# Kernel tuning notes

Hardware: AMD Instinct MI355X
Metric: run time of the kernel (lower is better)

Reference implementation:

```python
import jax, jax.numpy as jnp
import numpy as np

N_IN = 100000
N_OUT = 200000
C_IN = 128
C_OUT = 64
K = 27  # 3x3x3 kernel offsets
M = 100000  # neighbor-map pairs per kernel offset
BN_EPS = 1e-5


def setup_inputs() -> dict:
    key = jax.random.key(0)
    k1, k2, k3, k4 = jax.random.split(key, 4)
    x = jax.random.normal(k1, (N_IN, C_IN), dtype=jnp.float32)
    weight = jax.random.normal(k2, (K, C_IN, C_OUT), dtype=jnp.float32) * (1.0 / np.sqrt(C_IN * K))
    gamma = jnp.ones((C_OUT,), dtype=jnp.float32)
    beta = jnp.zeros((C_OUT,), dtype=jnp.float32)
    in_map = jax.random.randint(k3, (K, M), 0, N_IN, dtype=jnp.int32)
    out_map = jax.random.randint(k4, (K, M), 0, N_OUT, dtype=jnp.int32)
    return {"x": x, "weight": weight, "gamma": gamma, "beta": beta,
            "in_map": in_map, "out_map": out_map}


def sparse_transposed_conv(x, weight, in_map, out_map):
    # gather-GEMM-scatter over K kernel offsets (torchsparse semantics)
    out = jnp.zeros((N_OUT, C_OUT), dtype=x.dtype)

    def body(k, out):
        gathered = x[in_map[k]]                # [M, C_in] irregular gather
        contrib = gathered @ weight[k]         # [M, C_out] small GEMM
        return out.at[out_map[k]].add(contrib) # irregular scatter-add

    return jax.lax.fori_loop(0, K, body, out)


def reference(x, weight, gamma, beta, in_map, out_map):
    out = sparse_transposed_conv(x, weight, in_map, out_map)
    # BatchNorm over points (training-mode batch statistics, biased var)
    mean = jnp.mean(out, axis=0)
    var = jnp.mean(jnp.square(out - mean), axis=0)
    y = (out - mean) * (gamma * jax.lax.rsqrt(var + BN_EPS)) + beta
    return jnp.maximum(y, 0.0)  # ReLU
```

## Files before the change

### kernel.cpp

```cpp
#include <hip/hip_runtime.h>

#define N_IN   100000
#define N_OUT  200000
#define C_IN   128
#define C_OUT  64
#define NK     27
#define MM     100000
#define BN_EPS 1e-5f

#define TILE_M 128
#define APAD   136

typedef short bf16x8 __attribute__((ext_vector_type(8)));
typedef float f32x4  __attribute__((ext_vector_type(4)));

__device__ __forceinline__ unsigned pack2_bf16(float a, float b) {
  unsigned ua = __float_as_uint(a);
  unsigned ub = __float_as_uint(b);
  ua = (ua + 0x7FFFu + ((ua >> 16) & 1u)) >> 16;
  ub = (ub + 0x7FFFu + ((ub >> 16) & 1u)) & 0xFFFF0000u;
  return ua | ub;
}

__global__ void convert_wt_kernel(const float* __restrict__ w, unsigned* __restrict__ wt) {
  int pidx = blockIdx.x * 256 + threadIdx.x;
  int k   = pidx >> 12;
  int rem = pidx & 4095;
  int co  = rem >> 6;
  int ci0 = (rem & 63) * 2;
  const float* wk = w + (size_t)k * C_IN * C_OUT;
  float a = wk[ci0 * C_OUT + co];
  float b = wk[(ci0 + 1) * C_OUT + co];
  wt[pidx] = pack2_bf16(a, b);
}

__global__ __launch_bounds__(256) void scatter_kernel(
    const float* __restrict__ x,
    const unsigned short* __restrict__ wt,
    const int* __restrict__ in_map,
    const int* __restrict__ out_map,
    float* __restrict__ out)
{
  __shared__ unsigned short Als[TILE_M * APAD];
  __shared__ unsigned short Bls[C_OUT * APAD];
  __shared__ int om[TILE_M];

  const int t = threadIdx.x;
  const int k = blockIdx.y;
  const int mbase = blockIdx.x * TILE_M;

  if (t < TILE_M) {
    int m = mbase + t;
    om[t] = (m < MM) ? out_map[k * MM + m] : 0;
  }

  {
    const uint4* src = (const uint4*)(wt + (size_t)k * C_OUT * C_IN);
    #pragma unroll
    for (int i = 0; i < 4; ++i) {
      int ch  = t + i * 256;
      int co  = ch >> 4;
      int ci0 = (ch & 15) * 8;
      *(uint4*)&Bls[co * APAD + ci0] = src[ch];
    }
  }

  {
    int r    = t >> 1;
    int half = t & 1;
    int m    = mbase + r;
    int src  = (m < MM) ? in_map[k * MM + m] : 0;
    const float4* xr = (const float4*)(x + (size_t)src * C_IN) + half * 16;
    uint2* dst = (uint2*)&Als[r * APAD + half * 64];
    #pragma unroll
    for (int j = 0; j < 16; ++j) {
      float4 v = xr[j];
      dst[j] = make_uint2(pack2_bf16(v.x, v.y), pack2_bf16(v.z, v.w));
    }
  }
  __syncthreads();

  const int wave = t >> 6;
  const int lane = t & 63;
  const int quad = lane >> 4;
  const int l15  = lane & 15;
  const int rb   = wave * 32;

  f32x4 acc[2][4];
  #pragma unroll
  for (int i = 0; i < 2; ++i)
    #pragma unroll
    for (int j = 0; j < 4; ++j)
      acc[i][j] = (f32x4){0.f, 0.f, 0.f, 0.f};

  #pragma unroll
  for (int kk = 0; kk < 4; ++kk) {
    const int koff = kk * 32 + quad * 8;
    bf16x8 a0 = *(const bf16x8*)&Als[(rb + l15) * APAD + koff];
    bf16x8 a1 = *(const bf16x8*)&Als[(rb + 16 + l15) * APAD + koff];
    bf16x8 b0 = *(const bf16x8*)&Bls[(l15) * APAD + koff];
    bf16x8 b1 = *(const bf16x8*)&Bls[(16 + l15) * APAD + koff];
    bf16x8 b2 = *(const bf16x8*)&Bls[(32 + l15) * APAD + koff];
    bf16x8 b3 = *(const bf16x8*)&Bls[(48 + l15) * APAD + koff];
    acc[0][0] = __builtin_amdgcn_mfma_f32_16x16x32_bf16(a0, b0, acc[0][0], 0, 0, 0);
    acc[0][1] = __builtin_amdgcn_mfma_f32_16x16x32_bf16(a0, b1, acc[0][1], 0, 0, 0);
    acc[0][2] = __builtin_amdgcn_mfma_f32_16x16x32_bf16(a0, b2, acc[0][2], 0, 0, 0);
    acc[0][3] = __builtin_amdgcn_mfma_f32_16x16x32_bf16(a0, b3, acc[0][3], 0, 0, 0);
    acc[1][0] = __builtin_amdgcn_mfma_f32_16x16x32_bf16(a1, b0, acc[1][0], 0, 0, 0);
    acc[1][1] = __builtin_amdgcn_mfma_f32_16x16x32_bf16(a1, b1, acc[1][1], 0, 0, 0);
    acc[1][2] = __builtin_amdgcn_mfma_f32_16x16x32_bf16(a1, b2, acc[1][2], 0, 0, 0);
    acc[1][3] = __builtin_amdgcn_mfma_f32_16x16x32_bf16(a1, b3, acc[1][3], 0, 0, 0);
  }

  #pragma unroll
  for (int rt = 0; rt < 2; ++rt) {
    int rloc = rb + rt * 16 + quad * 4;
    int4 o4 = *(const int4*)&om[rloc];
    int mrow = mbase + rloc;
    #pragma unroll
    for (int ct = 0; ct < 4; ++ct) {
      f32x4 v = acc[rt][ct];
      int col = ct * 16 + l15;
      if (mrow + 0 < MM) unsafeAtomicAdd(&out[(size_t)o4.x * C_OUT + col], v[0]);
      if (mrow + 1 < MM) unsafeAtomicAdd(&out[(size_t)o4.y * C_OUT + col], v[1]);
      if (mrow + 2 < MM) unsafeAtomicAdd(&out[(size_t)o4.z * C_OUT + col], v[2]);
      if (mrow + 3 < MM) unsafeAtomicAdd(&out[(size_t)o4.w * C_OUT + col], v[3]);
    }
  }
}

__global__ void stats_kernel(const float* __restrict__ out, float* __restrict__ ws) {
  __shared__ float ls[4][64];
  __shared__ float ls2[4][64];
  int t = threadIdx.x;
  int c = t & 63, sub = t >> 6;
  float s = 0.f, s2 = 0.f;
  for (int r = blockIdx.x * 4 + sub; r < N_OUT; r += gridDim.x * 4) {
    float v = out[(size_t)r * C_OUT + c];
    s += v; s2 += v * v;
  }
  ls[sub][c] = s; ls2[sub][c] = s2;
  __syncthreads();
  if (t < 64) {
    float ts = ls[0][t] + ls[1][t] + ls[2][t] + ls[3][t];
    float t2 = ls2[0][t] + ls2[1][t] + ls2[2][t] + ls2[3][t];
    unsafeAtomicAdd(&ws[t], ts);
    unsafeAtomicAdd(&ws[64 + t], t2);
  }
}

__global__ void prep_kernel(float* __restrict__ ws,
                            const float* __restrict__ gamma,
                            const float* __restrict__ beta) {
  int c = threadIdx.x;
  float mean = ws[c] * (1.0f / N_OUT);
  float var  = ws[64 + c] * (1.0f / N_OUT) - mean * mean;
  var = fmaxf(var, 0.0f);
  float sc = gamma[c] * rsqrtf(var + BN_EPS);
  ws[128 + c] = sc;
  ws[192 + c] = beta[c] - mean * sc;
}

__global__ void finalize_kernel(float* __restrict__ out, const float* __restrict__ ws) {
  int i = blockIdx.x * 256 + threadIdx.x;
  float4 v = ((const float4*)out)[i];
  int c0 = (i & 15) * 4;
  float s0 = ws[128 + c0], s1 = ws[129 + c0], s2 = ws[130 + c0], s3 = ws[131 + c0];
  float b0 = ws[192 + c0], b1 = ws[193 + c0], b2 = ws[194 + c0], b3 = ws[195 + c0];
  v.x = fmaxf(fmaf(v.x, s0, b0), 0.f);
  v.y = fmaxf(fmaf(v.y, s1, b1), 0.f);
  v.z = fmaxf(fmaf(v.z, s2, b2), 0.f);
  v.w = fmaxf(fmaf(v.w, s3, b3), 0.f);
  ((float4*)out)[i] = v;
}

extern "C" void kernel_launch(void* const* d_in, const int* in_sizes, int n_in,
                              void* d_out, int out_size, void* d_ws, size_t ws_size,
                              hipStream_t stream) {
  const float* x      = (const float*)d_in[0];
  const float* weight = (const float*)d_in[1];
  const float* gamma  = (const float*)d_in[2];
  const float* beta   = (const float*)d_in[3];
  const int* in_map   = (const int*)d_in[4];
  const int* out_map  = (const int*)d_in[5];
  float* out   = (float*)d_out;
  float* stats = (float*)d_ws;
  unsigned* wt = (unsigned*)((char*)d_ws + 1024);

  hipMemsetAsync(d_out, 0, (size_t)N_OUT * C_OUT * sizeof(float), stream);
  hipMemsetAsync(d_ws, 0, 1024, stream);

  convert_wt_kernel<<<432, 256, 0, stream>>>(weight, wt);

  dim3 g((MM + TILE_M - 1) / TILE_M, NK);
  scatter_kernel<<<g, 256, 0, stream>>>(x, (const unsigned short*)wt, in_map, out_map, out);

  stats_kernel<<<512, 256, 0, stream>>>(out, stats);
  prep_kernel<<<1, 64, 0, stream>>>(stats, gamma, beta);
  finalize_kernel<<<(N_OUT * C_OUT / 4 + 255) / 256, 256, 0, stream>>>(out, stats);
}
```

Baseline: 735.6 us.

## Accumulate scatter output in fp16 with packed atomics into workspace buffer

Scatter-add now goes to an fp16 accumulation buffer in the workspace using packed global_atomic_pk_add_f16, pairing adjacent columns via lane shuffles. This halves the number of atomics and the bytes touched by the scatter, the memset, and the stats pass. The stats and finalize kernels are rewritten to read fp16 and write fp32 output. The risk is accumulation precision: summing many fp16 partials can lose accuracy or overflow versus fp32. The path runs only when the workspace is large enough.

```diff
diff --git a/kernel.cpp b/kernel.cpp
--- a/kernel.cpp
+++ b/kernel.cpp
@@ -1,4 +1,5 @@
 #include <hip/hip_runtime.h>
+#include <hip/hip_fp16.h>
 
 #define N_IN   100000
 #define N_OUT  200000
@@ -20,6 +21,16 @@
   ua = (ua + 0x7FFFu + ((ua >> 16) & 1u)) >> 16;
   ub = (ub + 0x7FFFu + ((ub >> 16) & 1u)) & 0xFFFF0000u;
   return ua | ub;
+}
+
+__device__ __forceinline__ unsigned pack2_f16(float lo, float hi) {
+  __half2 h = __floats2half2_rn(lo, hi);
+  return *(unsigned*)&h;
+}
+
+__device__ __forceinline__ void pk_atomic_f16(const void* addr, unsigned pw) {
+  asm volatile("global_atomic_pk_add_f16 %0, %1, off"
+               :: "v"((unsigned long long)addr), "v"(pw) : "memory");
 }
 
 __global__ void convert_wt_kernel(const float* __restrict__ w, unsigned* __restrict__ wt) {
@@ -34,12 +45,14 @@
   wt[pidx] = pack2_bf16(a, b);
 }
 
+template <bool F16>
 __global__ __launch_bounds__(256) void scatter_kernel(
     const float* __restrict__ x,
     const unsigned short* __restrict__ wt,
     const int* __restrict__ in_map,
     const int* __restrict__ out_map,
-    float* __restrict__ out)
+    float* __restrict__ outf,
+    unsigned short* __restrict__ acc16)
 {
   __shared__ unsigned short Als[TILE_M * APAD];
   __shared__ unsigned short Bls[C_OUT * APAD];
@@ -112,21 +125,93 @@
     acc[1][3] = __builtin_amdgcn_mfma_f32_16x16x32_bf16(a1, b3, acc[1][3], 0, 0, 0);
   }
 
-  #pragma unroll
-  for (int rt = 0; rt < 2; ++rt) {
-    int rloc = rb + rt * 16 + quad * 4;
-    int4 o4 = *(const int4*)&om[rloc];
-    int mrow = mbase + rloc;
-    #pragma unroll
-    for (int ct = 0; ct < 4; ++ct) {
-      f32x4 v = acc[rt][ct];
-      int col = ct * 16 + l15;
-      if (mrow + 0 < MM) unsafeAtomicAdd(&out[(size_t)o4.x * C_OUT + col], v[0]);
-      if (mrow + 1 < MM) unsafeAtomicAdd(&out[(size_t)o4.y * C_OUT + col], v[1]);
-      if (mrow + 2 < MM) unsafeAtomicAdd(&out[(size_t)o4.z * C_OUT + col], v[2]);
-      if (mrow + 3 < MM) unsafeAtomicAdd(&out[(size_t)o4.w * C_OUT + col], v[3]);
-    }
-  }
+  if constexpr (F16) {
+    const int par = l15 & 1;
+    #pragma unroll
+    for (int rt = 0; rt < 2; ++rt) {
+      int rloc = rb + rt * 16 + quad * 4;
+      int mrow = mbase + rloc;
+      #pragma unroll
+      for (int ct = 0; ct < 4; ++ct) {
+        f32x4 v = acc[rt][ct];
+        int colb = ct * 16 + (l15 & ~1);
+        #pragma unroll
+        for (int i = 0; i < 4; ++i) {
+          float vn = __shfl_xor(v[i], 1);
+          float lo = par ? vn : v[i];
+          float hi = par ? v[i] : vn;
+          unsigned pw = pack2_f16(lo, hi);
+          if (((i & 1) == par) && (mrow + i < MM)) {
+            const unsigned short* addr = acc16 + (size_t)om[rloc + i] * C_OUT + colb;
+            pk_atomic_f16(addr, pw);
+          }
+        }
+      }
+    }
+  } else {
+    #pragma unroll
+    for (int rt = 0; rt < 2; ++rt) {
+      int rloc = rb + rt * 16 + quad * 4;
+      int4 o4 = *(const int4*)&om[rloc];
+      int mrow = mbase + rloc;
+      #pragma unroll
+      for (int ct = 0; ct < 4; ++ct) {
+        f32x4 v = acc[rt][ct];
+        int col = ct * 16 + l15;
+        if (mrow + 0 < MM) unsafeAtomicAdd(&outf[(size_t)o4.x * C_OUT + col], v[0]);
+        if (mrow + 1 < MM) unsafeAtomicAdd(&outf[(size_t)o4.y * C_OUT + col], v[1]);
+        if (mrow + 2 < MM) unsafeAtomicAdd(&outf[(size_t)o4.z * C_OUT + col], v[2]);
+        if (mrow + 3 < MM) unsafeAtomicAdd(&outf[(size_t)o4.w * C_OUT + col], v[3]);
+      }
+    }
+  }
+}
+
+__global__ __launch_bounds__(256) void stats16_kernel(const unsigned* __restrict__ acc,
+                                                      float* __restrict__ ws) {
+  __shared__ float red[4][8][32];
+  int t = threadIdx.x;
+  int w = t & 31, sub = t >> 5;
+  float s0 = 0, q0 = 0, s1 = 0, q1 = 0;
+  for (int r = blockIdx.x * 8 + sub; r < N_OUT; r += gridDim.x * 8) {
+    unsigned u = acc[(size_t)r * 32 + w];
+    __half2 h = *(__half2*)&u;
+    float a = __low2float(h), b = __high2float(h);
+    s0 += a; q0 += a * a; s1 += b; q1 += b * b;
+  }
+  red[0][sub][w] = s0; red[1][sub][w] = q0;
+  red[2][sub][w] = s1; red[3][sub][w] = q1;
+  __syncthreads();
+  if (t < 32) {
+    float S0 = 0, Q0 = 0, S1 = 0, Q1 = 0;
+    #pragma unroll
+    for (int s = 0; s < 8; ++s) {
+      S0 += red[0][s][t]; Q0 += red[1][s][t];
+      S1 += red[2][s][t]; Q1 += red[3][s][t];
+    }
+    unsafeAtomicAdd(&ws[2 * t],      S0);
+    unsafeAtomicAdd(&ws[64 + 2 * t], Q0);
+    unsafeAtomicAdd(&ws[2 * t + 1],      S1);
+    unsafeAtomicAdd(&ws[64 + 2 * t + 1], Q1);
+  }
+}
+
+__global__ void finalize16_kernel(const uint2* __restrict__ acc,
+                                  float* __restrict__ out,
+                                  const float* __restrict__ ws) {
+  int i = blockIdx.x * 256 + threadIdx.x;
+  uint2 u = acc[i];
+  __half2 h0 = *(__half2*)&u.x;
+  __half2 h1 = *(__half2*)&u.y;
+  int c0 = (i & 15) * 4;
+  float s0 = ws[128 + c0], s1 = ws[129 + c0], s2 = ws[130 + c0], s3 = ws[131 + c0];
+  float b0 = ws[192 + c0], b1 = ws[193 + c0], b2 = ws[194 + c0], b3 = ws[195 + c0];
+  float4 v;
+  v.x = fmaxf(fmaf(__low2float(h0),  s0, b0), 0.f);
+  v.y = fmaxf(fmaf(__high2float(h0), s1, b1), 0.f);
+  v.z = fmaxf(fmaf(__low2float(h1),  s2, b2), 0.f);
+  v.w = fmaxf(fmaf(__high2float(h1), s3, b3), 0.f);
+  ((float4*)out)[i] = v;
 }
 
 __global__ void stats_kernel(const float* __restrict__ out, float* __restrict__ ws) {
@@ -147,18 +232,6 @@
     unsafeAtomicAdd(&ws[t], ts);
     unsafeAtomicAdd(&ws[64 + t], t2);
   }
-}
-
-__global__ void prep_kernel(float* __restrict__ ws,
-                            const float* __restrict__ gamma,
-                            const float* __restrict__ beta) {
-  int c = threadIdx.x;
-  float mean = ws[c] * (1.0f / N_OUT);
-  float var  = ws[64 + c] * (1.0f / N_OUT) - mean * mean;
-  var = fmaxf(var, 0.0f);
-  float sc = gamma[c] * rsqrtf(var + BN_EPS);
-  ws[128 + c] = sc;
-  ws[192 + c] = beta[c] - mean * sc;
 }
 
 __global__ void finalize_kernel(float* __restrict__ out, const float* __restrict__ ws) {
@@ -172,6 +245,18 @@
   v.z = fmaxf(fmaf(v.z, s2, b2), 0.f);
   v.w = fmaxf(fmaf(v.w, s3, b3), 0.f);
   ((float4*)out)[i] = v;
+}
+
+__global__ void prep_kernel(float* __restrict__ ws,
+                            const float* __restrict__ gamma,
+                            const float* __restrict__ beta) {
+  int c = threadIdx.x;
+  float mean = ws[c] * (1.0f / N_OUT);
+  float var  = ws[64 + c] * (1.0f / N_OUT) - mean * mean;
+  var = fmaxf(var, 0.0f);
+  float sc = gamma[c] * rsqrtf(var + BN_EPS);
+  ws[128 + c] = sc;
+  ws[192 + c] = beta[c] - mean * sc;
 }
 
 extern "C" void kernel_launch(void* const* d_in, const int* in_sizes, int n_in,
@@ -186,16 +271,29 @@
   float* out   = (float*)d_out;
   float* stats = (float*)d_ws;
   unsigned* wt = (unsigned*)((char*)d_ws + 1024);
-
-  hipMemsetAsync(d_out, 0, (size_t)N_OUT * C_OUT * sizeof(float), stream);
+  unsigned short* acc16 = (unsigned short*)((char*)d_ws + (1 << 20));
+
+  const size_t ACC_BYTES = (size_t)N_OUT * C_OUT * sizeof(unsigned short);
+  const bool f16path = ws_size >= ((1u << 20) + ACC_BYTES);
+
   hipMemsetAsync(d_ws, 0, 1024, stream);
-
   convert_wt_kernel<<<432, 256, 0, stream>>>(weight, wt);
 
   dim3 g((MM + TILE_M - 1) / TILE_M, NK);
-  scatter_kernel<<<g, 256, 0, stream>>>(x, (const unsigned short*)wt, in_map, out_map, out);
-
-  stats_kernel<<<512, 256, 0, stream>>>(out, stats);
-  prep_kernel<<<1, 64, 0, stream>>>(stats, gamma, beta);
-  finalize_kernel<<<(N_OUT * C_OUT / 4 + 255) / 256, 256, 0, stream>>>(out, stats);
-}
+  if (f16path) {
+    hipMemsetAsync(acc16, 0, ACC_BYTES, stream);
+    scatter_kernel<true><<<g, 256, 0, stream>>>(x, (const unsigned short*)wt,
+                                                in_map, out_map, out, acc16);
+    stats16_kernel<<<1024, 256, 0, stream>>>((const unsigned*)acc16, stats);
+    prep_kernel<<<1, 64, 0, stream>>>(stats, gamma, beta);
+    finalize16_kernel<<<(N_OUT * C_OUT / 4 + 255) / 256, 256, 0, stream>>>(
+        (const uint2*)acc16, out, stats);
+  } else {
+    hipMemsetAsync(d_out, 0, (size_t)N_OUT * C_OUT * sizeof(float), stream);
+    scatter_kernel<false><<<g, 256, 0, stream>>>(x, (const unsigned short*)wt,
+                                                 in_map, out_map, out, acc16);
+    stats_kernel<<<512, 256, 0, stream>>>(out, stats);
+    prep_kernel<<<1, 64, 0, stream>>>(stats, gamma, beta);
+    finalize_kernel<<<(N_OUT * C_OUT / 4 + 255) / 256, 256, 0, stream>>>(out, stats);
+  }
+}
```

After: 750.7 us. 1.02x slower.
